# Performance work log

Measured on AMD Instinct MI355X. Metric: run time of the kernel, lower is better.

The kernel has to match this reference:

```python
import jax, jax.numpy as jnp
import numpy as np

B, CIN, H, W = 8, 512, 32, 32
NH = 8
DQ = DK = DV = 256  # int(0.5 * Cin)
COUT = 512


def setup_inputs() -> dict:
    key = jax.random.key(0)
    k0, k1, k2, k3, k4 = jax.random.split(key, 5)
    x = jax.random.normal(k0, (B, CIN, H, W), dtype=jnp.float32)
    # 1x1 conv weights stored as [out, in] matrices (kernel size 1)
    w_qkv = jax.random.normal(k1, (DQ + DK + DV, CIN), dtype=jnp.float32) * 0.02
    b_qkv = jax.random.normal(k2, (DQ + DK + DV,), dtype=jnp.float32) * 0.02
    w_attn = jax.random.normal(k3, (COUT, DV), dtype=jnp.float32) * 0.02
    b_attn = jax.random.normal(k4, (COUT,), dtype=jnp.float32) * 0.02
    return {"x": x, "w_qkv": w_qkv, "b_qkv": b_qkv, "w_attn": w_attn, "b_attn": b_attn}


def _split_heads(t):
    b, c, h, w = t.shape
    return t.reshape(b, NH, c // NH, h, w)


def reference(x, w_qkv, b_qkv, w_attn, b_attn):
    b, _, h, w = x.shape
    hw = h * w
    # 1x1 conv == per-pixel GEMM
    qkv = jnp.einsum('bchw,oc->bohw', x, w_qkv) + b_qkv[None, :, None, None]
    q = qkv[:, :DQ]
    k = qkv[:, DQ:DQ + DK]
    v = qkv[:, DQ + DK:]
    dkh = DK // NH
    q = _split_heads(q) * (dkh ** -0.5)
    k = _split_heads(k)
    v = _split_heads(v)
    flat_q = q.reshape(b, NH, DQ // NH, hw)
    flat_k = k.reshape(b, NH, DK // NH, hw)
    flat_v = v.reshape(b, NH, DV // NH, hw)
    # logits: [b, NH, hw, hw]  (q^T k over feature dim)
    logits = jnp.einsum('bndq,bndk->bnqk', flat_q, flat_k)
    # FAITHFUL quirk: softmax over the HEAD axis (dim=1), as in the source
    weights = jax.nn.softmax(logits, axis=1)
    # attn_out: [b, NH, hw, dvh]
    attn_out = jnp.einsum('bnqk,bndk->bnqd', weights, flat_v)
    # FAITHFUL quirk: raw reshape (no transpose) to [b, NH, dvh, H, W]
    attn_out = attn_out.reshape(b, NH, DV // NH, h, w).reshape(b, DV, h, w)
    out = jnp.einsum('bchw,oc->bohw', attn_out, w_attn) + b_attn[None, :, None, None]
    return out
```

## Files before the change

### kernel.cpp

```cpp
#include <hip/hip_runtime.h>
#include <hip/hip_bf16.h>
#include <math.h>

#define BATCH 8
#define CIN   512
#define DQKV  768
#define NHEAD 8
#define HW    1024

typedef __attribute__((ext_vector_type(8))) short  short8;
typedef __attribute__((ext_vector_type(4))) float  float4v;

__device__ __forceinline__ ushort f2bf(float f) {
    union { float f; unsigned u; } c; c.f = f;
    unsigned u = c.u + 0x7fffu + ((c.u >> 16) & 1u);
    return (ushort)(u >> 16);
}

__device__ __forceinline__ uint pkbf(float a, float b) {
    union { __hip_bfloat162 h; uint u; } c;
    c.h = __float22bfloat162_rn(make_float2(a, b));
    return c.u;
}

__device__ __forceinline__ void async_ld16(const ushort* g, ushort* l) {
    auto gp = (const __attribute__((address_space(1))) unsigned int*)g;
    auto lp = (__attribute__((address_space(3))) unsigned int*)l;
    __builtin_amdgcn_global_load_lds(gp, lp, 16, 0, 0);
}

__global__ __launch_bounds__(256)
void transpose_cvt(const float* __restrict__ in, ushort* __restrict__ out,
                   int K, int N)
{
    __shared__ float Ts[64][65];
    const int b  = blockIdx.z;
    const int k0 = blockIdx.y * 64;
    const int n0 = blockIdx.x * 64;
    const int t  = threadIdx.x;
    const float* ib = in + (size_t)b * K * N;
    ushort*      ob = out + (size_t)b * N * K;

    const int r  = t >> 4;
    const int c4 = (t & 15) * 4;
    #pragma unroll
    for (int p = 0; p < 4; ++p) {
        float4 v = *(const float4*)(ib + (size_t)(k0 + r + 16 * p) * N + n0 + c4);
        Ts[r + 16 * p][c4 + 0] = v.x;
        Ts[r + 16 * p][c4 + 1] = v.y;
        Ts[r + 16 * p][c4 + 2] = v.z;
        Ts[r + 16 * p][c4 + 3] = v.w;
    }
    __syncthreads();

    const int nl = t >> 3;
    const int kc = (t & 7) * 8;
    #pragma unroll
    for (int p = 0; p < 2; ++p) {
        int n = nl + 32 * p;
        uint4 u;
        u.x = pkbf(Ts[kc + 0][n], Ts[kc + 1][n]);
        u.y = pkbf(Ts[kc + 2][n], Ts[kc + 3][n]);
        u.z = pkbf(Ts[kc + 4][n], Ts[kc + 5][n]);
        u.w = pkbf(Ts[kc + 6][n], Ts[kc + 7][n]);
        *(uint4*)(ob + (size_t)(n0 + n) * K + k0 + kc) = u;
    }
}

__global__ void cvt_bf16(const float* __restrict__ in, ushort* __restrict__ out, int n8)
{
    int i = blockIdx.x * blockDim.x + threadIdx.x;
    if (i >= n8) return;
    const float4* p = (const float4*)(in + (size_t)i * 8);
    float4 a = p[0], b = p[1];
    uint4 u;
    u.x = pkbf(a.x, a.y);
    u.y = pkbf(a.z, a.w);
    u.z = pkbf(b.x, b.y);
    u.w = pkbf(b.z, b.w);
    *(uint4*)(out + (size_t)i * 8) = u;
}

#define TEW 136

template<int M, int K, bool QSCALE, int OUTMODE>
__global__ __launch_bounds__(256, 2)
void gemm_bt(const ushort* __restrict__ A, const ushort* __restrict__ Bt,
             const float* __restrict__ bias, void* __restrict__ Oo,
             ushort* __restrict__ qt, ushort* __restrict__ kt)
{
    __shared__ __align__(16) ushort SH[16384];
    ushort* As = SH;
    ushort* Bs = SH + 8192;

    const int b    = blockIdx.z;
    const int m0   = blockIdx.y * 128;
    const int n0   = blockIdx.x * 128;
    const int t    = threadIdx.x;
    const int lane = t & 63;
    const int wave = t >> 6;
    const int l16  = lane & 15;
    const int quad = lane >> 4;
    const int wm   = (wave & 1) * 64;
    const int wn   = (wave >> 1) * 64;

    const ushort* Bb = Bt + (size_t)b * HW * K;

    float4v acc[4][4];
    #pragma unroll
    for (int i = 0; i < 4; ++i)
        #pragma unroll
        for (int j = 0; j < 4; ++j)
            acc[i][j] = (float4v){0.f, 0.f, 0.f, 0.f};

    const int srow = t >> 3;
    const int sg   = t & 7;

    for (int k0 = 0; k0 < K; k0 += 64) {
        __syncthreads();
        #pragma unroll
        for (int is = 0; is < 4; ++is) {
            int row = srow + is * 32;
            int gch = sg ^ (row & 7);
            async_ld16(A  + (size_t)(m0 + row) * K + k0 + gch * 8,
                       As + (size_t)t * 8 + is * 2048);
            async_ld16(Bb + (size_t)(n0 + row) * K + k0 + gch * 8,
                       Bs + (size_t)t * 8 + is * 2048);
        }
        __syncthreads();

        #pragma unroll
        for (int ks = 0; ks < 2; ++ks) {
            short8 af[4], bf[4];
            #pragma unroll
            for (int i = 0; i < 4; ++i) {
                int row = wm + i * 16 + l16;
                int ch  = (ks * 4 + quad) ^ (row & 7);
                af[i] = *(const short8*)&As[row * 64 + ch * 8];
            }
            #pragma unroll
            for (int j = 0; j < 4; ++j) {
                int row = wn + j * 16 + l16;
                int ch  = (ks * 4 + quad) ^ (row & 7);
                bf[j] = *(const short8*)&Bs[row * 64 + ch * 8];
            }
            #pragma unroll
            for (int i = 0; i < 4; ++i)
                #pragma unroll
                for (int j = 0; j < 4; ++j)
                    acc[i][j] = __builtin_amdgcn_mfma_f32_16x16x32_bf16(
                        af[i], bf[j], acc[i][j], 0, 0, 0);
        }
    }

    if (OUTMODE == 2 && m0 < 512) {
        ushort* dst = (m0 < 256) ? qt : kt;
        const int headbase = (m0 & 255) >> 5;
        const float sc = (QSCALE && m0 < 256) ? 0.17677669529663687f : 1.0f;
        #pragma unroll
        for (int hn = 0; hn < 2; ++hn) {
            __syncthreads();
            if ((wave >> 1) == hn) {
                #pragma unroll
                for (int i = 0; i < 4; ++i) {
                    int m_l = wm + i * 16 + quad * 4;
                    float bi[4];
                    #pragma unroll
                    for (int rr = 0; rr < 4; ++rr) bi[rr] = bias[m0 + m_l + rr];
                    #pragma unroll
                    for (int j = 0; j < 4; ++j) {
                        int n_l = j * 16 + l16;
                        uint2 pk;
                        pk.x = pkbf((acc[i][j][0] + bi[0]) * sc,
                                    (acc[i][j][1] + bi[1]) * sc);
                        pk.y = pkbf((acc[i][j][2] + bi[2]) * sc,
                                    (acc[i][j][3] + bi[3]) * sc);
                        *(uint2*)&SH[n_l * TEW + m_l] = pk;
                    }
                }
            }
            __syncthreads();
            #pragma unroll
            for (int p = 0; p < 4; ++p) {
                int idx = p * 256 + t;
                int d8 = idx & 3, h_l = (idx >> 2) & 3, n_l = idx >> 4;
                uint4 u = *(const uint4*)&SH[n_l * TEW + h_l * 32 + d8 * 8];
                size_t a = ((size_t)(b * NHEAD + headbase + h_l) * HW
                            + (n0 + hn * 64 + n_l)) * 32 + d8 * 8;
                *(uint4*)(dst + a) = u;
            }
        }
    } else {
        #pragma unroll
        for (int i = 0; i < 4; ++i) {
            #pragma unroll
            for (int rr = 0; rr < 4; ++rr) {
                int m = m0 + wm + i * 16 + quad * 4 + rr;
                float bi = bias[m];
                #pragma unroll
                for (int j = 0; j < 4; ++j) {
                    int n = n0 + wn + j * 16 + l16;
                    float val = acc[i][j][rr] + bi;
                    if (OUTMODE == 2)
                        ((ushort*)Oo)[((size_t)b * 256 + (m & 255)) * HW + n] = f2bf(val);
                    else
                        ((float*)Oo)[((size_t)b * M + m) * HW + n] = val;
                }
            }
        }
    }
}

#define WROW 136
#define OROW 132

__global__ __launch_bounds__(512, 4)
void attn_kernel(const ushort* __restrict__ vb, const ushort* __restrict__ Qt,
                 const ushort* __restrict__ Kt, ushort* __restrict__ ab)
{
    __shared__ __align__(16) ushort Ws[NHEAD * 16 * WROW];

    const int t    = threadIdx.x;
    const int b    = blockIdx.y;
    const int j    = blockIdx.x >> 1;
    const int uh   = blockIdx.x & 1;
    const int wave = t >> 6;
    const int lane = t & 63;
    const int l16  = lane & 15;
    const int quad = lane >> 4;

    const ushort* Vb  = vb + (size_t)b * 256 * HW;
    const ushort* Qtb = Qt + (size_t)b * (NHEAD * HW * 32);
    const ushort* Ktb = Kt + (size_t)b * (NHEAD * HW * 32);

    const int qlane = (uh * 16 + l16) * 32 + j;
    short8 qf[NHEAD];
    #pragma unroll
    for (int h = 0; h < NHEAD; ++h)
        qf[h] = *(const short8*)(Qtb + ((size_t)h * HW + qlane) * 32 + quad * 8);

    auto compute_wpk = [&](int k0, uint2* wpk) {
        const int kk = k0 + wave * 16 + l16;
        float4v S[NHEAD];
        #pragma unroll
        for (int h = 0; h < NHEAD; ++h) {
            short8 kf = *(const short8*)(Ktb + ((size_t)h * HW + kk) * 32 + quad * 8);
            S[h] = __builtin_amdgcn_mfma_f32_16x16x32_bf16(
                kf, qf[h], (float4v){0.f, 0.f, 0.f, 0.f}, 0, 0, 0);
        }
        float4v mx = S[0];
        #pragma unroll
        for (int h = 1; h < NHEAD; ++h)
            #pragma unroll
            for (int r = 0; r < 4; ++r) mx[r] = fmaxf(mx[r], S[h][r]);
        float4v sum = (float4v){0.f, 0.f, 0.f, 0.f};
        #pragma unroll
        for (int h = 0; h < NHEAD; ++h)
            #pragma unroll
            for (int r = 0; r < 4; ++r) {
                S[h][r] = __expf(S[h][r] - mx[r]);
                sum[r] += S[h][r];
            }
        float4v inv;
        #pragma unroll
        for (int r = 0; r < 4; ++r) inv[r] = __builtin_amdgcn_rcpf(sum[r]);
        #pragma unroll
        for (int h = 0; h < NHEAD; ++h) {
            wpk[h].x = pkbf(S[h][0] * inv[0], S[h][1] * inv[1]);
            wpk[h].y = pkbf(S[h][2] * inv[2], S[h][3] * inv[3]);
        }
    };

    float4v oacc[2];
    oacc[0] = (float4v){0.f, 0.f, 0.f, 0.f};
    oacc[1] = (float4v){0.f, 0.f, 0.f, 0.f};

    {
        uint2 w0[NHEAD];
        compute_wpk(0, w0);
        #pragma unroll
        for (int h = 0; h < NHEAD; ++h)
            *(uint2*)&Ws[(size_t)(h * 16 + l16) * WROW + wave * 16 + quad * 4] = w0[h];
    }
    __syncthreads();

    for (int i = 0; i < 8; ++i) {
        const int k0 = i * 128;

        uint2 nxt[NHEAD];
        if (i < 7) compute_wpk(k0 + 128, nxt);

        #pragma unroll
        for (int ks = 0; ks < 4; ++ks) {
            short8 wf = *(const short8*)&Ws[(size_t)(wave * 16 + l16) * WROW + ks * 32 + quad * 8];
            #pragma unroll
            for (int ds = 0; ds < 2; ++ds) {
                short8 vf = *(const short8*)(Vb + (size_t)(wave * 32 + ds * 16 + l16) * HW
                                             + k0 + ks * 32 + quad * 8);
                oacc[ds] = __builtin_amdgcn_mfma_f32_16x16x32_bf16(wf, vf, oacc[ds], 0, 0, 0);
            }
        }

        if (i < 7) {
            __syncthreads();
            #pragma unroll
            for (int h = 0; h < NHEAD; ++h)
                *(uint2*)&Ws[(size_t)(h * 16 + l16) * WROW + wave * 16 + quad * 4] = nxt[h];
            __syncthreads();
        }
    }

    __syncthreads();
    ushort* Ot = Ws;
    #pragma unroll
    for (int ds = 0; ds < 2; ++ds) {
        int d = ds * 16 + l16;
        #pragma unroll
        for (int r = 0; r < 4; ++r)
            Ot[(size_t)d * OROW + wave * 16 + quad * 4 + r] = f2bf(oacc[ds][r]);
    }
    __syncthreads();

    {
        int d  = t >> 4;
        int c8 = (t & 15) * 8;
        uint2 a = *(const uint2*)&Ot[(size_t)d * OROW + c8];
        uint2 b2 = *(const uint2*)&Ot[(size_t)d * OROW + c8 + 4];
        int h   = c8 >> 4;
        int col = h * 32 + uh * 16 + (c8 & 15);
        uint4 u = make_uint4(a.x, a.y, b2.x, b2.y);
        *(uint4*)(ab + ((size_t)b * HW + j * 32 + d) * 256 + col) = u;
    }
}

extern "C" void kernel_launch(void* const* d_in, const int* in_sizes, int n_in,
                              void* d_out, int out_size, void* d_ws, size_t ws_size,
                              hipStream_t stream)
{
    const float* x      = (const float*)d_in[0];
    const float* w_qkv  = (const float*)d_in[1];
    const float* b_qkv  = (const float*)d_in[2];
    const float* w_attn = (const float*)d_in[3];
    const float* b_attn = (const float*)d_in[4];
    float* out = (float*)d_out;

    ushort* vb  = (ushort*)d_ws;
    ushort* xb  = vb + 2097152;
    ushort* Qt  = xb + 4194304;
    ushort* Kt  = Qt + 2097152;
    ushort* ab  = Kt + 2097152;
    ushort* wb1 = ab + 2097152;
    ushort* wb2 = wb1 + 393216;

    cvt_bf16<<<192, 256, 0, stream>>>(w_qkv, wb1, 49152);
    cvt_bf16<<<64, 256, 0, stream>>>(w_attn, wb2, 16384);
    transpose_cvt<<<dim3(16, 8, BATCH), 256, 0, stream>>>(x, xb, CIN, HW);

    gemm_bt<DQKV, CIN, true, 2>
        <<<dim3(8, 6, BATCH), 256, 0, stream>>>(wb1, xb, b_qkv, vb, Qt, Kt);

    attn_kernel<<<dim3(64, BATCH), 512, 0, stream>>>(vb, Qt, Kt, ab);

    gemm_bt<512, 256, false, 0>
        <<<dim3(8, 4, BATCH), 256, 0, stream>>>(wb2, ab, b_attn, out, nullptr, nullptr);
}
```

Before: 156.7 us.

## Split attention over key halves with fp32 partials and separate reduce kernel

The attention kernel now launches twice as many blocks, each processing half of the key range, so more work runs in parallel on the GPU. Each block writes fp32 partial outputs to a workspace buffer aliased over the no-longer-needed bf16 input copy. A new kernel sums the two halves and converts the result to bf16 for the output projection. The trade-off is extra global memory traffic for the partials and an extra launch, plus a higher launch-bounds occupancy hint that may constrain registers.

```diff
diff --git a/kernel.cpp b/kernel.cpp
--- a/kernel.cpp
+++ b/kernel.cpp
@@ -212,22 +212,24 @@
 }
 
 #define WROW 136
-#define OROW 132
-
-__global__ __launch_bounds__(512, 4)
+#define OROWF 132
+
+__global__ __launch_bounds__(512, 8)
 void attn_kernel(const ushort* __restrict__ vb, const ushort* __restrict__ Qt,
-                 const ushort* __restrict__ Kt, ushort* __restrict__ ab)
+                 const ushort* __restrict__ Kt, float* __restrict__ pb)
 {
     __shared__ __align__(16) ushort Ws[NHEAD * 16 * WROW];
 
     const int t    = threadIdx.x;
     const int b    = blockIdx.y;
+    const int s    = blockIdx.z;
     const int j    = blockIdx.x >> 1;
     const int uh   = blockIdx.x & 1;
     const int wave = t >> 6;
     const int lane = t & 63;
     const int l16  = lane & 15;
     const int quad = lane >> 4;
+    const int kbase = s * 512;
 
     const ushort* Vb  = vb + (size_t)b * 256 * HW;
     const ushort* Qtb = Qt + (size_t)b * (NHEAD * HW * 32);
@@ -277,18 +279,18 @@
 
     {
         uint2 w0[NHEAD];
-        compute_wpk(0, w0);
+        compute_wpk(kbase, w0);
         #pragma unroll
         for (int h = 0; h < NHEAD; ++h)
             *(uint2*)&Ws[(size_t)(h * 16 + l16) * WROW + wave * 16 + quad * 4] = w0[h];
     }
     __syncthreads();
 
-    for (int i = 0; i < 8; ++i) {
-        const int k0 = i * 128;
+    for (int i = 0; i < 4; ++i) {
+        const int k0 = kbase + i * 128;
 
         uint2 nxt[NHEAD];
-        if (i < 7) compute_wpk(k0 + 128, nxt);
+        if (i < 3) compute_wpk(k0 + 128, nxt);
 
         #pragma unroll
         for (int ks = 0; ks < 4; ++ks) {
@@ -301,7 +303,7 @@
             }
         }
 
-        if (i < 7) {
+        if (i < 3) {
             __syncthreads();
             #pragma unroll
             for (int h = 0; h < NHEAD; ++h)
@@ -311,26 +313,40 @@
     }
 
     __syncthreads();
-    ushort* Ot = Ws;
+    float* Ot = (float*)Ws;
     #pragma unroll
     for (int ds = 0; ds < 2; ++ds) {
         int d = ds * 16 + l16;
-        #pragma unroll
-        for (int r = 0; r < 4; ++r)
-            Ot[(size_t)d * OROW + wave * 16 + quad * 4 + r] = f2bf(oacc[ds][r]);
+        *(float4*)&Ot[(size_t)d * OROWF + wave * 16 + quad * 4] =
+            make_float4(oacc[ds][0], oacc[ds][1], oacc[ds][2], oacc[ds][3]);
     }
     __syncthreads();
 
-    {
-        int d  = t >> 4;
-        int c8 = (t & 15) * 8;
-        uint2 a = *(const uint2*)&Ot[(size_t)d * OROW + c8];
-        uint2 b2 = *(const uint2*)&Ot[(size_t)d * OROW + c8 + 4];
-        int h   = c8 >> 4;
-        int col = h * 32 + uh * 16 + (c8 & 15);
-        uint4 u = make_uint4(a.x, a.y, b2.x, b2.y);
-        *(uint4*)(ab + ((size_t)b * HW + j * 32 + d) * 256 + col) = u;
-    }
+    #pragma unroll
+    for (int p = 0; p < 2; ++p) {
+        int idx = p * 512 + t;
+        int d  = idx >> 5;
+        int u  = idx & 31;
+        int h  = u >> 2;
+        int c4 = (u & 3) * 4;
+        float4 v = *(const float4*)&Ot[(size_t)d * OROWF + h * 16 + c4];
+        size_t addr = (((size_t)s * BATCH + b) * HW + j * 32 + d) * 256
+                    + h * 32 + uh * 16 + c4;
+        *(float4*)(pb + addr) = v;
+    }
+}
+
+__global__ __launch_bounds__(512)
+void reduce_ab(const float* __restrict__ pb, ushort* __restrict__ ab)
+{
+    const size_t n = (size_t)BATCH * HW * 256;
+    size_t i = ((size_t)blockIdx.x * 512 + threadIdx.x) * 4;
+    float4 a = *(const float4*)(pb + i);
+    float4 b = *(const float4*)(pb + n + i);
+    uint2 u;
+    u.x = pkbf(a.x + b.x, a.y + b.y);
+    u.y = pkbf(a.z + b.z, a.w + b.w);
+    *(uint2*)(ab + i) = u;
 }
 
 extern "C" void kernel_launch(void* const* d_in, const int* in_sizes, int n_in,
@@ -345,12 +361,13 @@
     float* out = (float*)d_out;
 
     ushort* vb  = (ushort*)d_ws;
-    ushort* xb  = vb + 2097152;
-    ushort* Qt  = xb + 4194304;
+    ushort* Qt  = vb + 2097152;
     ushort* Kt  = Qt + 2097152;
     ushort* ab  = Kt + 2097152;
     ushort* wb1 = ab + 2097152;
     ushort* wb2 = wb1 + 393216;
+    ushort* xb  = wb2 + 131072;
+    float*  pb  = (float*)xb;
 
     cvt_bf16<<<192, 256, 0, stream>>>(w_qkv, wb1, 49152);
     cvt_bf16<<<64, 256, 0, stream>>>(w_attn, wb2, 16384);
@@ -359,7 +376,9 @@
     gemm_bt<DQKV, CIN, true, 2>
         <<<dim3(8, 6, BATCH), 256, 0, stream>>>(wb1, xb, b_qkv, vb, Qt, Kt);
 
-    attn_kernel<<<dim3(64, BATCH), 512, 0, stream>>>(vb, Qt, Kt, ab);
+    attn_kernel<<<dim3(64, BATCH, 2), 512, 0, stream>>>(vb, Qt, Kt, pb);
+
+    reduce_ab<<<1024, 512, 0, stream>>>(pb, ab);
 
     gemm_bt<512, 256, false, 0>
         <<<dim3(8, 4, BATCH), 256, 0, stream>>>(wb2, ab, b_attn, out, nullptr, nullptr);
```

Result: slower. 185.7 us (+18.5%).
